# Kernel optimization log

Hardware: AMD Instinct MI355X
Metric: run time of the kernel (lower is better)

Reference implementation:

```python
import jax, jax.numpy as jnp
import numpy as np

H = 256   # hidden_dim
K = 4     # number of z_layer Linears
T = 8192  # number of permutation trees (Z-nodes) in the batch
C = 16    # children (leaf indices) per tree
N = 200000  # rows in batch.x node-feature table


def setup_inputs() -> dict:
    key = jax.random.key(0)
    ks = jax.random.split(key, 6)
    x = jax.random.normal(ks[0], (N, H), dtype=jnp.float32)
    leaf_idx = jax.random.randint(ks[1], (T, C), 0, N)
    # z_layer: k Linears (y = x @ W + b), z_final_layer: one Linear
    scale = 1.0 / np.sqrt(H)
    Wz = jax.random.uniform(ks[2], (K, H, H), dtype=jnp.float32, minval=-scale, maxval=scale)
    bz = jax.random.uniform(ks[3], (K, H), dtype=jnp.float32, minval=-scale, maxval=scale)
    Wzf = jax.random.uniform(ks[4], (H, H), dtype=jnp.float32, minval=-scale, maxval=scale)
    bzf = jax.random.uniform(ks[5], (H,), dtype=jnp.float32, minval=-scale, maxval=scale)
    return {"x": x, "Wz": Wz, "bz": bz, "Wzf": Wzf, "bzf": bzf, "leaf_idx": leaf_idx}


def reference(x, Wz, bz, Wzf, bzf, leaf_idx):
    # Batched z_layer_fn over T trees, each a Z-node over C leaf children.
    data = x[leaf_idx]                                   # [T, C, H] gather (fetch_or_produce)
    # k parallel Linears: [K, T, C, H]
    after = jnp.einsum('tch,khd->ktcd', data, Wz) + bz[:, None, None, :]
    # embedding_k[torch.roll(arange(C), shifts=k)] == roll(embedding_k, k, axis=children)
    k = after.shape[0]
    rolled_sum = after[0]
    for i in range(1, k):  # tiny fixed loop over k layers
        rolled_sum = rolled_sum + jnp.roll(after[i], i, axis=1)
    h = jax.nn.elu(rolled_sum)                           # [T, C, H]
    h = jnp.einsum('tch,hd->tcd', h, Wzf) + bzf          # z_final_layer
    out = jax.nn.elu(jnp.sum(h, axis=1))                 # sum over children, ELU -> [T, H]
    return out
```

## Files before the change

### kernel.cpp

```cpp
#include <hip/hip_runtime.h>
#include <stdint.h>

#define TREES 8192
#define HID   256
#define CH    16
#define KL    4
#define G     8
#define NG    2
#define GB    (G * NG)
#define LDSS  264

typedef short bf16x8 __attribute__((ext_vector_type(8)));
typedef float f32x4  __attribute__((ext_vector_type(4)));

__device__ __forceinline__ unsigned short f2bf(float f) {
    unsigned u = __builtin_bit_cast(unsigned, f);
    u += 0x7FFFu + ((u >> 16) & 1u);
    return (unsigned short)(u >> 16);
}
__device__ __forceinline__ float elu1(float x) {
    return x > 0.f ? x : (__expf(x) - 1.f);
}
__device__ __forceinline__ uint4 pack8(float4 a, float4 b) {
    union { uint4 u4; unsigned short s[8]; } U;
    U.s[0] = f2bf(a.x); U.s[1] = f2bf(a.y); U.s[2] = f2bf(a.z); U.s[3] = f2bf(a.w);
    U.s[4] = f2bf(b.x); U.s[5] = f2bf(b.y); U.s[6] = f2bf(b.z); U.s[7] = f2bf(b.w);
    return U.u4;
}

__global__ void prep_transpose(const float* __restrict__ Wz,
                               const float* __restrict__ Wzf,
                               const float* __restrict__ bz,
                               unsigned short* __restrict__ WzT,
                               unsigned short* __restrict__ WzfT,
                               float* __restrict__ bzsum) {
    __shared__ unsigned short ts[64][65];
    const int k  = blockIdx.z;
    const int h0 = blockIdx.x * 64;
    const int d0 = blockIdx.y * 64;
    const float* src = (k < KL) ? (Wz + (k << 16)) : Wzf;
    unsigned short* dst = (k < KL) ? (WzT + (k << 16)) : WzfT;
    const int tid = threadIdx.x;
    const int jc  = tid & 63;
    #pragma unroll
    for (int r = 0; r < 16; ++r) {
        int i = r * 4 + (tid >> 6);
        ts[jc][i] = f2bf(src[(h0 + i) * HID + d0 + jc]);
    }
    __syncthreads();
    #pragma unroll
    for (int r = 0; r < 16; ++r) {
        int jl = r * 4 + (tid >> 6);
        dst[(d0 + jl) * HID + h0 + jc] = ts[jl][jc];
    }
    if (k == KL && blockIdx.x == 0 && blockIdx.y == 0) {
        float s = 0.f;
        #pragma unroll
        for (int kk = 0; kk < KL; ++kk) s += bz[kk * HID + tid];
        bzsum[tid] = s;
    }
}

__global__ __launch_bounds__(256, 2) void ptree_kernel(
    const float* __restrict__ x,
    const int* __restrict__ leaf,
    const float* __restrict__ bzf,
    const unsigned short* __restrict__ WzT,
    const unsigned short* __restrict__ WzfT,
    const float* __restrict__ bzsum,
    float* __restrict__ out,
    int nrows)
{
    __shared__ __align__(16) unsigned short sh[G][CH][LDSS];
    __shared__ __align__(16) unsigned short hs[GB][LDSS];
    const int tid  = threadIdx.x;
    const int lane = tid & 63;
    const int wave = tid >> 6;
    const int t0   = blockIdx.x * GB;
    const int ncol = lane & 15;
    const int quad = lane >> 4;

    float bzs[4], bzfv[4];
    #pragma unroll
    for (int nt = 0; nt < 4; ++nt) {
        bzs[nt]  = bzsum[wave * 64 + nt * 16 + ncol];
        bzfv[nt] = bzf[wave * 64 + nt * 16 + ncol];
    }

    const unsigned short* wz_base = WzT + (wave * 64 + ncol) * HID + quad * 8;

    for (int grp = 0; grp < NG; ++grp) {
        const int tg = t0 + grp * G;

        #pragma unroll
        for (int i = 0; i < (G * CH * 32) / 256; ++i) {
            int cid = i * 256 + tid;
            int g   = cid >> 9;
            int row = (cid >> 5) & 15;
            int ch  = cid & 31;
            int idx = leaf[(tg + g) * CH + row];
            idx = ((unsigned)idx < (unsigned)nrows) ? idx : 0;
            const float* src = x + (size_t)idx * HID + ch * 8;
            float4 v0 = *(const float4*)src;
            float4 v1 = *(const float4*)(src + 4);
            *(uint4*)&sh[g][row][ch * 8] = pack8(v0, v1);
        }

        __syncthreads();

        f32x4 acc1[G][4];
        #pragma unroll
        for (int g = 0; g < G; ++g)
            #pragma unroll
            for (int nt = 0; nt < 4; ++nt) acc1[g][nt] = f32x4{0.f, 0.f, 0.f, 0.f};

        bf16x8 bc[4], bn[4];
        #pragma unroll
        for (int nt = 0; nt < 4; ++nt)
            bc[nt] = *(const bf16x8*)(wz_base + nt * 16 * HID);

        #pragma unroll 2
        for (int s = 0; s < KL * 8; ++s) {
            const int sn = (s < KL * 8 - 1) ? s + 1 : s;
            const unsigned short* pn = wz_base + (sn >> 3) * 65536 + (sn & 7) * 32;
            #pragma unroll
            for (int nt = 0; nt < 4; ++nt)
                bn[nt] = *(const bf16x8*)(pn + nt * 16 * HID);
            const int k    = s >> 3;
            const int kt   = s & 7;
            const int arow = (ncol - k) & 15;
            #pragma unroll
            for (int g = 0; g < G; ++g) {
                bf16x8 a = *(const bf16x8*)&sh[g][arow][kt * 32 + quad * 8];
                #pragma unroll
                for (int nt = 0; nt < 4; ++nt)
                    acc1[g][nt] = __builtin_amdgcn_mfma_f32_16x16x32_bf16(
                        a, bc[nt], acc1[g][nt], 0, 0, 0);
            }
            #pragma unroll
            for (int nt = 0; nt < 4; ++nt) bc[nt] = bn[nt];
        }

        #pragma unroll
        for (int g = 0; g < G; ++g)
            #pragma unroll
            for (int nt = 0; nt < 4; ++nt) {
                float sv = 0.f;
                #pragma unroll
                for (int r = 0; r < 4; ++r) sv += elu1(acc1[g][nt][r] + bzs[nt]);
                sv += __shfl_xor(sv, 16);
                sv += __shfl_xor(sv, 32);
                if (quad == 0) hs[grp * G + g][wave * 64 + nt * 16 + ncol] = f2bf(sv);
            }

        __syncthreads();
    }

    f32x4 acc2[4];
    #pragma unroll
    for (int nt = 0; nt < 4; ++nt) acc2[nt] = f32x4{0.f, 0.f, 0.f, 0.f};

    const unsigned short* wzf_base = WzfT + (wave * 64 + ncol) * HID + quad * 8;
    #pragma unroll 2
    for (int kt = 0; kt < 8; ++kt) {
        bf16x8 a = *(const bf16x8*)&hs[ncol][kt * 32 + quad * 8];
        #pragma unroll
        for (int nt = 0; nt < 4; ++nt) {
            bf16x8 b = *(const bf16x8*)(wzf_base + nt * 16 * HID + kt * 32);
            acc2[nt] = __builtin_amdgcn_mfma_f32_16x16x32_bf16(a, b, acc2[nt], 0, 0, 0);
        }
    }

    #pragma unroll
    for (int nt = 0; nt < 4; ++nt)
        #pragma unroll
        for (int r = 0; r < 4; ++r) {
            const int tree = quad * 4 + r;
            float v = elu1(acc2[nt][r] + 16.f * bzfv[nt]);
            out[(size_t)(t0 + tree) * HID + wave * 64 + nt * 16 + ncol] = v;
        }
}

extern "C" void kernel_launch(void* const* d_in, const int* in_sizes, int n_in,
                              void* d_out, int out_size, void* d_ws, size_t ws_size,
                              hipStream_t stream) {
    (void)out_size; (void)ws_size;
    const void* p_x = nullptr; const void* p_Wz = nullptr; const void* p_bz = nullptr;
    const void* p_Wzf = nullptr; const void* p_bzf = nullptr; const void* p_leaf = nullptr;
    for (int i = 0; i < n_in; ++i) {
        switch (in_sizes[i]) {
            case 200000 * 256:   p_x    = d_in[i]; break;
            case KL * 256 * 256: p_Wz   = d_in[i]; break;
            case KL * 256:       p_bz   = d_in[i]; break;
            case 256 * 256:      p_Wzf  = d_in[i]; break;
            case 256:            p_bzf  = d_in[i]; break;
            case TREES * CH:     p_leaf = d_in[i]; break;
        }
    }
    const float* x    = (const float*)p_x;
    const float* Wz   = (const float*)p_Wz;
    const float* bz   = (const float*)p_bz;
    const float* Wzf  = (const float*)p_Wzf;
    const float* bzf  = (const float*)p_bzf;
    const int*   leaf = (const int*)p_leaf;

    unsigned short* WzT  = (unsigned short*)d_ws;
    unsigned short* WzfT = WzT + KL * HID * HID;
    float*          bzsum = (float*)(WzfT + HID * HID);

    dim3 tg(4, 4, KL + 1);
    prep_transpose<<<tg, 256, 0, stream>>>(Wz, Wzf, bz, WzT, WzfT, bzsum);
    ptree_kernel<<<TREES / GB, 256, 0, stream>>>(x, leaf, bzf, WzT, WzfT, bzsum,
                                                 (float*)d_out, 200000);
}
```

Before: 342.1 us.

## Warp-specialize kernel: producer waves prefetch gathers into double-buffered LDS while MFMA waves compute

Measured after the change: 359.4 us. 5.1% more time.

```diff
diff --git a/kernel.cpp b/kernel.cpp
--- a/kernel.cpp
+++ b/kernel.cpp
@@ -6,8 +6,8 @@
 #define CH    16
 #define KL    4
 #define G     8
-#define NG    2
-#define GB    (G * NG)
+#define NC    4
+#define GB    (G * NC)
 #define LDSS  264
 
 typedef short bf16x8 __attribute__((ext_vector_type(8)));
@@ -61,7 +61,7 @@
     }
 }
 
-__global__ __launch_bounds__(256, 2) void ptree_kernel(
+__global__ __launch_bounds__(512, 2) void ptree_kernel(
     const float* __restrict__ x,
     const int* __restrict__ leaf,
     const float* __restrict__ bzf,
@@ -71,7 +71,7 @@
     float* __restrict__ out,
     int nrows)
 {
-    __shared__ __align__(16) unsigned short sh[G][CH][LDSS];
+    __shared__ __align__(16) unsigned short sh[2][G][CH][LDSS];
     __shared__ __align__(16) unsigned short hs[GB][LDSS];
     const int tid  = threadIdx.x;
     const int lane = tid & 63;
@@ -79,106 +79,129 @@
     const int t0   = blockIdx.x * GB;
     const int ncol = lane & 15;
     const int quad = lane >> 4;
+    const int dbase = (wave & 3) * 64;
+
+    #pragma unroll
+    for (int i = 0; i < (G * CH * 32) / 512; ++i) {
+        int cid = i * 512 + tid;
+        int g   = cid >> 9;
+        int row = (cid >> 5) & 15;
+        int ch  = cid & 31;
+        int idx = leaf[(t0 + g) * CH + row];
+        idx = ((unsigned)idx < (unsigned)nrows) ? idx : 0;
+        const float* src = x + (size_t)idx * HID + ch * 8;
+        float4 v0 = *(const float4*)src;
+        float4 v1 = *(const float4*)(src + 4);
+        *(uint4*)&sh[0][g][row][ch * 8] = pack8(v0, v1);
+    }
 
     float bzs[4], bzfv[4];
     #pragma unroll
     for (int nt = 0; nt < 4; ++nt) {
-        bzs[nt]  = bzsum[wave * 64 + nt * 16 + ncol];
-        bzfv[nt] = bzf[wave * 64 + nt * 16 + ncol];
-    }
-
-    const unsigned short* wz_base = WzT + (wave * 64 + ncol) * HID + quad * 8;
-
-    for (int grp = 0; grp < NG; ++grp) {
-        const int tg = t0 + grp * G;
-
+        bzs[nt]  = bzsum[dbase + nt * 16 + ncol];
+        bzfv[nt] = bzf[dbase + nt * 16 + ncol];
+    }
+
+    const unsigned short* wz_base = WzT + (dbase + ncol) * HID + quad * 8;
+
+    __syncthreads();
+
+    for (int c = 0; c < NC; ++c) {
+        if (wave < 4) {
+            f32x4 acc1[G][4];
+            #pragma unroll
+            for (int g = 0; g < G; ++g)
+                #pragma unroll
+                for (int nt = 0; nt < 4; ++nt) acc1[g][nt] = f32x4{0.f, 0.f, 0.f, 0.f};
+
+            bf16x8 bc[4], bn[4];
+            #pragma unroll
+            for (int nt = 0; nt < 4; ++nt)
+                bc[nt] = *(const bf16x8*)(wz_base + nt * 16 * HID);
+
+            __builtin_amdgcn_s_setprio(1);
+            #pragma unroll 2
+            for (int s = 0; s < KL * 8; ++s) {
+                const int sn = (s < KL * 8 - 1) ? s + 1 : s;
+                const unsigned short* pn = wz_base + (sn >> 3) * 65536 + (sn & 7) * 32;
+                #pragma unroll
+                for (int nt = 0; nt < 4; ++nt)
+                    bn[nt] = *(const bf16x8*)(pn + nt * 16 * HID);
+                const int k    = s >> 3;
+                const int kt   = s & 7;
+                const int arow = (ncol - k) & 15;
+                #pragma unroll
+                for (int g = 0; g < G; ++g) {
+                    bf16x8 a = *(const bf16x8*)&sh[c & 1][g][arow][kt * 32 + quad * 8];
+                    #pragma unroll
+                    for (int nt = 0; nt < 4; ++nt)
+                        acc1[g][nt] = __builtin_amdgcn_mfma_f32_16x16x32_bf16(
+                            a, bc[nt], acc1[g][nt], 0, 0, 0);
+                }
+                #pragma unroll
+                for (int nt = 0; nt < 4; ++nt) bc[nt] = bn[nt];
+            }
+            __builtin_amdgcn_s_setprio(0);
+
+            #pragma unroll
+            for (int g = 0; g < G; ++g)
+                #pragma unroll
+                for (int nt = 0; nt < 4; ++nt) {
+                    float sv = 0.f;
+                    #pragma unroll
+                    for (int r = 0; r < 4; ++r) sv += elu1(acc1[g][nt][r] + bzs[nt]);
+                    sv += __shfl_xor(sv, 16);
+                    sv += __shfl_xor(sv, 32);
+                    if (quad == 0) hs[c * G + g][dbase + nt * 16 + ncol] = f2bf(sv);
+                }
+        } else if (c + 1 < NC) {
+            const int ptid = tid & 255;
+            const int tg   = t0 + (c + 1) * G;
+            #pragma unroll
+            for (int i = 0; i < (G * CH * 32) / 256; ++i) {
+                int cid = i * 256 + ptid;
+                int g   = cid >> 9;
+                int row = (cid >> 5) & 15;
+                int ch  = cid & 31;
+                int idx = leaf[(tg + g) * CH + row];
+                idx = ((unsigned)idx < (unsigned)nrows) ? idx : 0;
+                const float* src = x + (size_t)idx * HID + ch * 8;
+                float4 v0 = *(const float4*)src;
+                float4 v1 = *(const float4*)(src + 4);
+                *(uint4*)&sh[(c + 1) & 1][g][row][ch * 8] = pack8(v0, v1);
+            }
+        }
+        __syncthreads();
+    }
+
+    if (wave < 4) {
+        const unsigned short* wzf_base = WzfT + (dbase + ncol) * HID + quad * 8;
         #pragma unroll
-        for (int i = 0; i < (G * CH * 32) / 256; ++i) {
-            int cid = i * 256 + tid;
-            int g   = cid >> 9;
-            int row = (cid >> 5) & 15;
-            int ch  = cid & 31;
-            int idx = leaf[(tg + g) * CH + row];
-            idx = ((unsigned)idx < (unsigned)nrows) ? idx : 0;
-            const float* src = x + (size_t)idx * HID + ch * 8;
-            float4 v0 = *(const float4*)src;
-            float4 v1 = *(const float4*)(src + 4);
-            *(uint4*)&sh[g][row][ch * 8] = pack8(v0, v1);
+        for (int t2 = 0; t2 < 2; ++t2) {
+            f32x4 acc2[4];
+            #pragma unroll
+            for (int nt = 0; nt < 4; ++nt) acc2[nt] = f32x4{0.f, 0.f, 0.f, 0.f};
+
+            #pragma unroll 2
+            for (int kt = 0; kt < 8; ++kt) {
+                bf16x8 a = *(const bf16x8*)&hs[t2 * 16 + ncol][kt * 32 + quad * 8];
+                #pragma unroll
+                for (int nt = 0; nt < 4; ++nt) {
+                    bf16x8 b = *(const bf16x8*)(wzf_base + nt * 16 * HID + kt * 32);
+                    acc2[nt] = __builtin_amdgcn_mfma_f32_16x16x32_bf16(
+                        a, b, acc2[nt], 0, 0, 0);
+                }
+            }
+            #pragma unroll
+            for (int nt = 0; nt < 4; ++nt)
+                #pragma unroll
+                for (int r = 0; r < 4; ++r) {
+                    const int tree = t2 * 16 + quad * 4 + r;
+                    float v = elu1(acc2[nt][r] + 16.f * bzfv[nt]);
+                    out[(size_t)(t0 + tree) * HID + dbase + nt * 16 + ncol] = v;
+                }
         }
-
-        __syncthreads();
-
-        f32x4 acc1[G][4];
-        #pragma unroll
-        for (int g = 0; g < G; ++g)
-            #pragma unroll
-            for (int nt = 0; nt < 4; ++nt) acc1[g][nt] = f32x4{0.f, 0.f, 0.f, 0.f};
-
-        bf16x8 bc[4], bn[4];
-        #pragma unroll
-        for (int nt = 0; nt < 4; ++nt)
-            bc[nt] = *(const bf16x8*)(wz_base + nt * 16 * HID);
-
-        #pragma unroll 2
-        for (int s = 0; s < KL * 8; ++s) {
-            const int sn = (s < KL * 8 - 1) ? s + 1 : s;
-            const unsigned short* pn = wz_base + (sn >> 3) * 65536 + (sn & 7) * 32;
-            #pragma unroll
-            for (int nt = 0; nt < 4; ++nt)
-                bn[nt] = *(const bf16x8*)(pn + nt * 16 * HID);
-            const int k    = s >> 3;
-            const int kt   = s & 7;
-            const int arow = (ncol - k) & 15;
-            #pragma unroll
-            for (int g = 0; g < G; ++g) {
-                bf16x8 a = *(const bf16x8*)&sh[g][arow][kt * 32 + quad * 8];
-                #pragma unroll
-                for (int nt = 0; nt < 4; ++nt)
-                    acc1[g][nt] = __builtin_amdgcn_mfma_f32_16x16x32_bf16(
-                        a, bc[nt], acc1[g][nt], 0, 0, 0);
-            }
-            #pragma unroll
-            for (int nt = 0; nt < 4; ++nt) bc[nt] = bn[nt];
-        }
-
-        #pragma unroll
-        for (int g = 0; g < G; ++g)
-            #pragma unroll
-            for (int nt = 0; nt < 4; ++nt) {
-                float sv = 0.f;
-                #pragma unroll
-                for (int r = 0; r < 4; ++r) sv += elu1(acc1[g][nt][r] + bzs[nt]);
-                sv += __shfl_xor(sv, 16);
-                sv += __shfl_xor(sv, 32);
-                if (quad == 0) hs[grp * G + g][wave * 64 + nt * 16 + ncol] = f2bf(sv);
-            }
-
-        __syncthreads();
-    }
-
-    f32x4 acc2[4];
-    #pragma unroll
-    for (int nt = 0; nt < 4; ++nt) acc2[nt] = f32x4{0.f, 0.f, 0.f, 0.f};
-
-    const unsigned short* wzf_base = WzfT + (wave * 64 + ncol) * HID + quad * 8;
-    #pragma unroll 2
-    for (int kt = 0; kt < 8; ++kt) {
-        bf16x8 a = *(const bf16x8*)&hs[ncol][kt * 32 + quad * 8];
-        #pragma unroll
-        for (int nt = 0; nt < 4; ++nt) {
-            bf16x8 b = *(const bf16x8*)(wzf_base + nt * 16 * HID + kt * 32);
-            acc2[nt] = __builtin_amdgcn_mfma_f32_16x16x32_bf16(a, b, acc2[nt], 0, 0, 0);
-        }
-    }
-
-    #pragma unroll
-    for (int nt = 0; nt < 4; ++nt)
-        #pragma unroll
-        for (int r = 0; r < 4; ++r) {
-            const int tree = quad * 4 + r;
-            float v = elu1(acc2[nt][r] + 16.f * bzfv[nt]);
-            out[(size_t)(t0 + tree) * HID + wave * 64 + nt * 16 + ncol] = v;
-        }
+    }
 }
 
 extern "C" void kernel_launch(void* const* d_in, const int* in_sizes, int n_in,
@@ -210,6 +233,6 @@
 
     dim3 tg(4, 4, KL + 1);
     prep_transpose<<<tg, 256, 0, stream>>>(Wz, Wzf, bz, WzT, WzfT, bzsum);
-    ptree_kernel<<<TREES / GB, 256, 0, stream>>>(x, leaf, bzf, WzT, WzfT, bzsum,
+    ptree_kernel<<<TREES / GB, 512, 0, stream>>>(x, leaf, bzf, WzT, WzfT, bzsum,
                                                  (float*)d_out, 200000);
 }
```

## Split gather into separate kernel and double-buffer bf16 tiles via global_load_lds

Applied to the files above, without the earlier changes.

New measurement: 364.2 us. 6.5% more time.

```diff
diff --git a/kernel.cpp b/kernel.cpp
--- a/kernel.cpp
+++ b/kernel.cpp
@@ -26,6 +26,11 @@
     U.s[0] = f2bf(a.x); U.s[1] = f2bf(a.y); U.s[2] = f2bf(a.z); U.s[3] = f2bf(a.w);
     U.s[4] = f2bf(b.x); U.s[5] = f2bf(b.y); U.s[6] = f2bf(b.z); U.s[7] = f2bf(b.w);
     return U.u4;
+}
+__device__ __forceinline__ void gload_lds16(const void* g, void* l) {
+    __builtin_amdgcn_global_load_lds(
+        (const __attribute__((address_space(1))) void*)g,
+        (__attribute__((address_space(3))) void*)l, 16, 0, 0);
 }
 
 __global__ void prep_transpose(const float* __restrict__ Wz,
@@ -61,15 +66,152 @@
     }
 }
 
-__global__ __launch_bounds__(256, 2) void ptree_kernel(
-    const float* __restrict__ x,
-    const int* __restrict__ leaf,
+__global__ __launch_bounds__(256) void gather_kernel(
+    const float* __restrict__ x, const int* __restrict__ leaf,
+    unsigned short* __restrict__ dataB, int nrows)
+{
+    const int cid = blockIdx.x * 256 + threadIdx.x;
+    const int halfidx = cid >> 11;
+    const int w    = cid & 2047;
+    const int gg   = w >> 8;
+    const int ch2  = (w >> 4) & 15;
+    const int row  = w & 15;
+    const int t    = (halfidx >> 1) * 8 + gg;
+    const int ch   = (halfidx & 1) * 16 + ch2;
+    int idx = leaf[t * CH + row];
+    idx = ((unsigned)idx < (unsigned)nrows) ? idx : 0;
+    const float* src = x + (size_t)idx * HID + ch * 8;
+    float4 v0 = *(const float4*)src;
+    float4 v1 = *(const float4*)(src + 4);
+    *(uint4*)&dataB[(size_t)cid * 8] = pack8(v0, v1);
+}
+
+__global__ __launch_bounds__(256, 2) void ptree_pipe(
+    const unsigned short* __restrict__ dataB,
     const float* __restrict__ bzf,
     const unsigned short* __restrict__ WzT,
     const unsigned short* __restrict__ WzfT,
     const float* __restrict__ bzsum,
-    float* __restrict__ out,
-    int nrows)
+    float* __restrict__ out)
+{
+    __shared__ __align__(16) unsigned short shH[2][16384];
+    __shared__ __align__(16) unsigned short hs[GB][LDSS];
+    const int tid  = threadIdx.x;
+    const int lane = tid & 63;
+    const int wave = tid >> 6;
+    const int ncol = lane & 15;
+    const int quad = lane >> 4;
+    const int t0   = blockIdx.x * GB;
+
+    const size_t hbase = (size_t)blockIdx.x * 4 * 16384;
+
+    #pragma unroll
+    for (int i = 0; i < 8; ++i) {
+        const int c2 = i * 256 + tid;
+        gload_lds16(dataB + hbase + c2 * 8, &shH[0][c2 * 8]);
+    }
+
+    float bzs[4], bzfv[4];
+    #pragma unroll
+    for (int nt = 0; nt < 4; ++nt) {
+        bzs[nt]  = bzsum[wave * 64 + nt * 16 + ncol];
+        bzfv[nt] = bzf[wave * 64 + nt * 16 + ncol];
+    }
+
+    const unsigned short* wz_base = WzT + (wave * 64 + ncol) * HID + quad * 8;
+    bf16x8 bc[4], bn[4];
+    #pragma unroll
+    for (int nt = 0; nt < 4; ++nt)
+        bc[nt] = *(const bf16x8*)(wz_base + nt * 16 * HID);
+
+    __syncthreads();
+
+    f32x4 acc[G][4];
+    for (int half = 0; half < 4; ++half) {
+        const int hb = half & 1;
+        if (!(half & 1)) {
+            #pragma unroll
+            for (int g = 0; g < G; ++g)
+                #pragma unroll
+                for (int nt = 0; nt < 4; ++nt) acc[g][nt] = f32x4{0.f, 0.f, 0.f, 0.f};
+        }
+        if (half < 3) {
+            const size_t nb = hbase + (size_t)(half + 1) * 16384;
+            #pragma unroll
+            for (int i = 0; i < 8; ++i) {
+                const int c2 = i * 256 + tid;
+                gload_lds16(dataB + nb + c2 * 8, &shH[hb ^ 1][c2 * 8]);
+            }
+        }
+        #pragma unroll 2
+        for (int st = 0; st < 16; ++st) {
+            const int S  = half * 16 + st;
+            const int Sn = (S < 63) ? S + 1 : S;
+            const unsigned short* pn =
+                wz_base + ((Sn >> 2) & 3) * 65536 + (((Sn >> 4) & 1) * 4 + (Sn & 3)) * 32;
+            #pragma unroll
+            for (int nt = 0; nt < 4; ++nt)
+                bn[nt] = *(const bf16x8*)(pn + nt * 16 * HID);
+            const int k    = (S >> 2) & 3;
+            const int ktl  = S & 3;
+            const int arow = (ncol - k) & 15;
+            const int abase = (ktl * 4 + quad) * 128 + arow * 8;
+            #pragma unroll
+            for (int g = 0; g < G; ++g) {
+                bf16x8 a = *(const bf16x8*)&shH[hb][g * 2048 + abase];
+                #pragma unroll
+                for (int nt = 0; nt < 4; ++nt)
+                    acc[g][nt] = __builtin_amdgcn_mfma_f32_16x16x32_bf16(
+                        a, bc[nt], acc[g][nt], 0, 0, 0);
+            }
+            #pragma unroll
+            for (int nt = 0; nt < 4; ++nt) bc[nt] = bn[nt];
+        }
+        if (half & 1) {
+            const int grp = half >> 1;
+            #pragma unroll
+            for (int g = 0; g < G; ++g)
+                #pragma unroll
+                for (int nt = 0; nt < 4; ++nt) {
+                    float sv = 0.f;
+                    #pragma unroll
+                    for (int r = 0; r < 4; ++r) sv += elu1(acc[g][nt][r] + bzs[nt]);
+                    sv += __shfl_xor(sv, 16);
+                    sv += __shfl_xor(sv, 32);
+                    if (quad == 0) hs[grp * G + g][wave * 64 + nt * 16 + ncol] = f2bf(sv);
+                }
+        }
+        __syncthreads();
+    }
+
+    f32x4 acc2[4];
+    #pragma unroll
+    for (int nt = 0; nt < 4; ++nt) acc2[nt] = f32x4{0.f, 0.f, 0.f, 0.f};
+    const unsigned short* wzf_base = WzfT + (wave * 64 + ncol) * HID + quad * 8;
+    #pragma unroll 2
+    for (int kt = 0; kt < 8; ++kt) {
+        bf16x8 a = *(const bf16x8*)&hs[ncol][kt * 32 + quad * 8];
+        #pragma unroll
+        for (int nt = 0; nt < 4; ++nt) {
+            bf16x8 b = *(const bf16x8*)(wzf_base + nt * 16 * HID + kt * 32);
+            acc2[nt] = __builtin_amdgcn_mfma_f32_16x16x32_bf16(a, b, acc2[nt], 0, 0, 0);
+        }
+    }
+    #pragma unroll
+    for (int nt = 0; nt < 4; ++nt)
+        #pragma unroll
+        for (int r = 0; r < 4; ++r) {
+            const int tree = quad * 4 + r;
+            float v = elu1(acc2[nt][r] + 16.f * bzfv[nt]);
+            out[(size_t)(t0 + tree) * HID + wave * 64 + nt * 16 + ncol] = v;
+        }
+}
+
+__global__ __launch_bounds__(256, 2) void ptree_kernel(
+    const float* __restrict__ x, const int* __restrict__ leaf,
+    const float* __restrict__ bzf, const unsigned short* __restrict__ WzT,
+    const unsigned short* __restrict__ WzfT, const float* __restrict__ bzsum,
+    float* __restrict__ out, int nrows)
 {
     __shared__ __align__(16) unsigned short sh[G][CH][LDSS];
     __shared__ __align__(16) unsigned short hs[GB][LDSS];
@@ -86,12 +228,10 @@
         bzs[nt]  = bzsum[wave * 64 + nt * 16 + ncol];
         bzfv[nt] = bzf[wave * 64 + nt * 16 + ncol];
     }
-
     const unsigned short* wz_base = WzT + (wave * 64 + ncol) * HID + quad * 8;
 
     for (int grp = 0; grp < NG; ++grp) {
         const int tg = t0 + grp * G;
-
         #pragma unroll
         for (int i = 0; i < (G * CH * 32) / 256; ++i) {
             int cid = i * 256 + tid;
@@ -105,7 +245,6 @@
             float4 v1 = *(const float4*)(src + 4);
             *(uint4*)&sh[g][row][ch * 8] = pack8(v0, v1);
         }
-
         __syncthreads();
 
         f32x4 acc1[G][4];
@@ -152,14 +291,12 @@
                 sv += __shfl_xor(sv, 32);
                 if (quad == 0) hs[grp * G + g][wave * 64 + nt * 16 + ncol] = f2bf(sv);
             }
-
         __syncthreads();
     }
 
     f32x4 acc2[4];
     #pragma unroll
     for (int nt = 0; nt < 4; ++nt) acc2[nt] = f32x4{0.f, 0.f, 0.f, 0.f};
-
     const unsigned short* wzf_base = WzfT + (wave * 64 + ncol) * HID + quad * 8;
     #pragma unroll 2
     for (int kt = 0; kt < 8; ++kt) {
@@ -170,7 +307,6 @@
             acc2[nt] = __builtin_amdgcn_mfma_f32_16x16x32_bf16(a, b, acc2[nt], 0, 0, 0);
         }
     }
-
     #pragma unroll
     for (int nt = 0; nt < 4; ++nt)
         #pragma unroll
@@ -184,7 +320,7 @@
 extern "C" void kernel_launch(void* const* d_in, const int* in_sizes, int n_in,
                               void* d_out, int out_size, void* d_ws, size_t ws_size,
                               hipStream_t stream) {
-    (void)out_size; (void)ws_size;
+    (void)out_size;
     const void* p_x = nullptr; const void* p_Wz = nullptr; const void* p_bz = nullptr;
     const void* p_Wzf = nullptr; const void* p_bzf = nullptr; const void* p_leaf = nullptr;
     for (int i = 0; i < n_in; ++i) {
@@ -204,12 +340,25 @@
     const float* bzf  = (const float*)p_bzf;
     const int*   leaf = (const int*)p_leaf;
 
-    unsigned short* WzT  = (unsigned short*)d_ws;
-    unsigned short* WzfT = WzT + KL * HID * HID;
-    float*          bzsum = (float*)(WzfT + HID * HID);
+    const size_t dataB_shorts = (size_t)TREES * CH * HID;
+    const size_t needA = dataB_shorts * 2 + 524288 + 131072 + 1024;
 
     dim3 tg(4, 4, KL + 1);
-    prep_transpose<<<tg, 256, 0, stream>>>(Wz, Wzf, bz, WzT, WzfT, bzsum);
-    ptree_kernel<<<TREES / GB, 256, 0, stream>>>(x, leaf, bzf, WzT, WzfT, bzsum,
-                                                 (float*)d_out, 200000);
-}
+    if (ws_size >= needA) {
+        unsigned short* dataB = (unsigned short*)d_ws;
+        unsigned short* WzT   = dataB + dataB_shorts;
+        unsigned short* WzfT  = WzT + KL * HID * HID;
+        float*          bzsum = (float*)(WzfT + HID * HID);
+        prep_transpose<<<tg, 256, 0, stream>>>(Wz, Wzf, bz, WzT, WzfT, bzsum);
+        gather_kernel<<<(TREES * CH * 32) / 256, 256, 0, stream>>>(x, leaf, dataB, 200000);
+        ptree_pipe<<<TREES / GB, 256, 0, stream>>>(dataB, bzf, WzT, WzfT, bzsum,
+                                                   (float*)d_out);
+    } else {
+        unsigned short* WzT   = (unsigned short*)d_ws;
+        unsigned short* WzfT  = WzT + KL * HID * HID;
+        float*          bzsum = (float*)(WzfT + HID * HID);
+        prep_transpose<<<tg, 256, 0, stream>>>(Wz, Wzf, bz, WzT, WzfT, bzsum);
+        ptree_kernel<<<TREES / GB, 256, 0, stream>>>(x, leaf, bzf, WzT, WzfT, bzsum,
+                                                     (float*)d_out, 200000);
+    }
+}
```
